# Optimization experiments

Measured on AMD Instinct MI355X. Metric: run time of the kernel, lower is better.

## Reference

```python
import jax, jax.numpy as jnp
import numpy as np

H_HEADS = 8
DIM_HEAD = 64


def setup_inputs() -> dict:
    key = jax.random.key(0)
    ks = jax.random.split(key, 5)
    b, c, Hs, Ws = 16, 32, 128, 128
    qd = H_HEADS * c              # 256 (heads*c = Linear in_features)
    inner = H_HEADS * DIM_HEAD    # 512
    s = 0.02                      # keep logits in a sane range
    return {
        "x": jax.random.normal(ks[0], (b, c, Hs, Ws), jnp.float32),
        "Wq": jax.random.normal(ks[1], (inner, qd), jnp.float32) * s,
        "Wkv": jax.random.normal(ks[2], (2 * inner, qd), jnp.float32) * s,
        "Wout": jax.random.normal(ks[3], (qd, inner), jnp.float32) * s,
        "bout": jax.random.normal(ks[4], (qd,), jnp.float32) * s,
    }


def _proj(arg, W, bias=None):
    # apply_operator_or_ffn for nn.Linear:
    # rearrange '(b h) n d -> b d (h n)', Linear over last dim, then 'b d n -> b n d'
    B, n, d = arg.shape
    bp = B // H_HEADS
    t = arg.reshape(bp, H_HEADS, n, d)
    t = jnp.transpose(t, (0, 3, 1, 2)).reshape(bp, d, H_HEADS * n)  # [b', d, h*n]
    y = t @ W.T
    if bias is not None:
        y = y + bias
    return jnp.transpose(y, (0, 2, 1))  # [b', out_features, d]


def _split_heads(t):
    # 'b (h d) n -> (b h) d n'
    bp, hd, n = t.shape
    return t.reshape(bp, H_HEADS, hd // H_HEADS, n).reshape(bp * H_HEADS, hd // H_HEADS, n)


def reference(x, Wq, Wkv, Wout, bout):
    b, c = x.shape[0], x.shape[1]
    spatial = x.shape[2:]
    N = int(np.prod(spatial))
    scale = DIM_HEAD ** -0.5
    xf = x.reshape(b, c, N)
    q = _proj(xf, Wq)              # [b/h, inner, N]
    kv = _proj(xf, Wkv)            # [b/h, 2*inner, N]
    inner = q.shape[1]
    k, v = kv[:, :inner], kv[:, inner:]
    qh, kh, vh = _split_heads(q), _split_heads(k), _split_heads(v)  # [b, DIM_HEAD, N]
    sim = jnp.einsum('bin,bjn->bij', qh, kh) * scale                 # [b, dh, dh]
    attn = jax.nn.softmax(sim, axis=-1)
    out = jnp.einsum('bnj,bjd->bnd', attn, vh)                       # [b, dh, N]
    out = _proj(out, Wout, bout)                                     # [b/h, h*c, N]
    return out.reshape(b, c, *spatial)
```

## Files before the change

### kernel.cpp

```cpp
#include <hip/hip_runtime.h>
#include <cstdint>
#include <cstddef>

using u16 = unsigned short;
using u32 = unsigned int;

typedef __attribute__((ext_vector_type(8))) short bf16x8;
typedef __attribute__((ext_vector_type(16))) float f32x16;

__device__ __forceinline__ u16 f2bf(float f) {
  union { float f; u32 i; } x; x.f = f;
  u32 r = (x.i + 0x7FFFu + ((x.i >> 16) & 1u)) >> 16;
  return (u16)r;
}
__device__ __forceinline__ bf16x8 ldbf16x8(const u16* p) {
  union { uint4 u; bf16x8 v; } t;
  t.u = *(const uint4*)p;
  return t.v;
}

constexpr int NP = 16384;


constexpr size_t OFF_C   = 0;
constexpr size_t OFF_T   = 131072;
constexpr size_t OFF_AT  = 393216;
constexpr size_t OFF_WE  = 458752;
constexpr size_t OFF_MT  = 720896;
constexpr size_t OFF_MA  = 851968;
constexpr size_t OFF_XB  = 917504;
constexpr size_t OFF_XBT = 5111808;
constexpr size_t OFF_CP1 = 9306112;
constexpr size_t NEED1   = (OFF_CP1 + 2097152) * 4;
constexpr size_t OFF_CP2 = 851968;
constexpr size_t NEED2   = (OFF_CP2 + 6291456) * 4;

__global__ __launch_bounds__(256)
void k0_cvt(const float* __restrict__ x, u16* __restrict__ XbF,
            u16* __restrict__ XbTF) {
  __shared__ float Fs[256 * 65];
  const int pc = blockIdx.x;
  const int g  = blockIdx.y;
  const int p0 = pc * 64;
  const float* __restrict__ Xg = x + (size_t)g * 256 * NP;
  u16* __restrict__ XbFg  = XbF  + (size_t)g * 256 * NP;
  u16* __restrict__ XbTFg = XbTF + (size_t)g * NP * 256;
  const int tid = threadIdx.x;
  const int f8i = tid & 7, rb = tid >> 3;
  const int sA = pc * 4 + (f8i >> 1);
  const int hA = f8i & 1;
  for (int pass = 0; pass < 8; ++pass) {
    const int row = rb + pass * 32;
    const size_t e0 = (size_t)row * NP + p0 + f8i * 8;
    float4 a = *(const float4*)(Xg + e0);
    float4 b = *(const float4*)(Xg + e0 + 4);
    const float v[8] = {a.x, a.y, a.z, a.w, b.x, b.y, b.z, b.w};
    uint4 s;
    s.x = (u32)f2bf(v[0]) | ((u32)f2bf(v[1]) << 16);
    s.y = (u32)f2bf(v[2]) | ((u32)f2bf(v[3]) << 16);
    s.z = (u32)f2bf(v[4]) | ((u32)f2bf(v[5]) << 16);
    s.w = (u32)f2bf(v[6]) | ((u32)f2bf(v[7]) << 16);
    const int panel = row >> 5, lc = row & 31;
    *(uint4*)(XbFg + (size_t)panel * 524288 + sA * 512 + hA * 256 + lc * 8) = s;
    float* d = &Fs[row * 65 + f8i * 8];
#pragma unroll
    for (int e = 0; e < 8; ++e) d[e] = v[e];
  }
  __syncthreads();
  const int p = tid & 63, grp = tid >> 6;
  const int pp = p0 + p;
  const int panelT = pp >> 5, lcT = pp & 31;
  u16* dstT = XbTFg + (size_t)panelT * 8192 + lcT * 8;
  for (int c = 0; c < 4; ++c) {
    const int sT = grp * 4 + c;
    u32 w[8];
#pragma unroll
    for (int q = 0; q < 8; ++q) {
      const int f = grp * 64 + c * 16 + q * 2;
      u32 lo = f2bf(Fs[f * 65 + p]);
      u32 hi = f2bf(Fs[(f + 1) * 65 + p]);
      w[q] = lo | (hi << 16);
    }
    uint4 s0 = {w[0], w[1], w[2], w[3]};
    uint4 s1 = {w[4], w[5], w[6], w[7]};
    *(uint4*)(dstT + sT * 512)       = s0;
    *(uint4*)(dstT + sT * 512 + 256) = s1;
  }
}

__global__ __launch_bounds__(256)
void k1_mfma(const u16* __restrict__ XbF, float* __restrict__ Cpart) {
  const int kc = blockIdx.x;
  const int tp = blockIdx.y;
  const int g  = blockIdx.z;
  const int ti = tp >> 2, tj = tp & 3;
  const int tid = threadIdx.x;
  const int w = tid >> 6, half = (tid >> 5) & 1, lc = tid & 31;
  const int qi = w >> 1, qj = w & 1;
  const u16* __restrict__ Xg = XbF + (size_t)g * 256 * NP;
  const u16* A = Xg + (size_t)(ti * 2 + qi) * 524288 + (size_t)kc * 32768 +
                 half * 256 + lc * 8;
  const u16* B = Xg + (size_t)(tj * 2 + qj) * 524288 + (size_t)kc * 32768 +
                 half * 256 + lc * 8;
  f32x16 acc;
#pragma unroll
  for (int i = 0; i < 16; ++i) acc[i] = 0.f;
#pragma unroll 4
  for (int s = 0; s < 64; ++s) {
    bf16x8 a = ldbf16x8(A + s * 512);
    bf16x8 b = ldbf16x8(B + s * 512);
    acc = __builtin_amdgcn_mfma_f32_32x32x16_bf16(a, b, acc, 0, 0, 0);
  }
  float* __restrict__ P = Cpart + (((size_t)g * 16 + tp) * 16 + kc) * 4096;
#pragma unroll
  for (int r = 0; r < 16; ++r) {
    const int row = qi * 32 + (r & 3) + 8 * (r >> 2) + 4 * half;
    const int col = qj * 32 + lc;
    P[row * 64 + col] = acc[r];
  }
}

__global__ __launch_bounds__(256)
void k1b_red(const float* __restrict__ Cpart, float* __restrict__ Cmat) {
  const int sl = blockIdx.x;
  const int tp = blockIdx.y;
  const int g  = blockIdx.z;
  const int ele = sl * 256 + threadIdx.x;
  const float* __restrict__ P =
      Cpart + (((size_t)g * 16 + tp) * 16) * 4096 + ele;
  float v = 0.f;
#pragma unroll
  for (int kc = 0; kc < 16; ++kc) v += P[(size_t)kc * 4096];
  const int ti = tp >> 2, tj = tp & 3;
  const int r64 = ele >> 6, c64 = ele & 63;
  Cmat[(size_t)g * 65536 + (size_t)(ti * 64 + r64) * 256 + tj * 64 + c64] = v;
}

__global__ __launch_bounds__(256)
void k1_gram(const float* __restrict__ x, float* __restrict__ Cpart) {
  __shared__ float As[32 * 132];
  __shared__ float Bs[32 * 132];
  const int kc = blockIdx.x, ty = blockIdx.y, g = blockIdx.z;
  const int i0 = (ty == 2) ? 128 : 0;
  const int j0 = (ty == 0) ? 0 : 128;
  const float* __restrict__ Xg = x + (size_t)g * 256 * NP;
  const int tid = threadIdx.x, lane = tid & 63, w = tid >> 6;
  const int wy = (w >> 1) * 64, wx = (w & 1) * 64;
  const int ly = (lane >> 3) * 8, lx = (lane & 7) * 8;
  float acc[8][8];
#pragma unroll
  for (int e = 0; e < 8; ++e)
#pragma unroll
    for (int f = 0; f < 8; ++f) acc[e][f] = 0.f;
  const int k8 = (tid & 3) * 8, rowb = tid >> 2, k0 = kc * 256;
  for (int s = 0; s < 8; ++s) {
    const int ks = k0 + s * 32;
#pragma unroll
    for (int pass = 0; pass < 2; ++pass) {
      const int row = rowb + pass * 64;
      const size_t ea = (size_t)(i0 + row) * NP + ks + k8;
      float4 a = *(const float4*)(Xg + ea);
      float4 b = *(const float4*)(Xg + ea + 4);
      As[(k8+0)*132+row]=a.x; As[(k8+1)*132+row]=a.y;
      As[(k8+2)*132+row]=a.z; As[(k8+3)*132+row]=a.w;
      As[(k8+4)*132+row]=b.x; As[(k8+5)*132+row]=b.y;
      As[(k8+6)*132+row]=b.z; As[(k8+7)*132+row]=b.w;
      const size_t eb = (size_t)(j0 + row) * NP + ks + k8;
      a = *(const float4*)(Xg + eb);
      b = *(const float4*)(Xg + eb + 4);
      Bs[(k8+0)*132+row]=a.x; Bs[(k8+1)*132+row]=a.y;
      Bs[(k8+2)*132+row]=a.z; Bs[(k8+3)*132+row]=a.w;
      Bs[(k8+4)*132+row]=b.x; Bs[(k8+5)*132+row]=b.y;
      Bs[(k8+6)*132+row]=b.z; Bs[(k8+7)*132+row]=b.w;
    }
    __syncthreads();
#pragma unroll 4
    for (int kk = 0; kk < 32; ++kk) {
      const float* ar = &As[kk * 132 + wy + ly];
      const float* br = &Bs[kk * 132 + wx + lx];
      float4 a0 = *(const float4*)(ar), a1 = *(const float4*)(ar + 4);
      float4 b0 = *(const float4*)(br), b1 = *(const float4*)(br + 4);
      const float av[8] = {a0.x,a0.y,a0.z,a0.w,a1.x,a1.y,a1.z,a1.w};
      const float bv[8] = {b0.x,b0.y,b0.z,b0.w,b1.x,b1.y,b1.z,b1.w};
#pragma unroll
      for (int e = 0; e < 8; ++e)
#pragma unroll
        for (int f = 0; f < 8; ++f) acc[e][f] += av[e] * bv[f];
    }
    __syncthreads();
  }
  float* __restrict__ P = Cpart + (((size_t)g * 3 + ty) * 64 + kc) * 16384;
#pragma unroll
  for (int e = 0; e < 8; ++e) {
    float* pr = P + (size_t)(wy + ly + e) * 128 + wx + lx;
    float4 s0 = {acc[e][0], acc[e][1], acc[e][2], acc[e][3]};
    float4 s1 = {acc[e][4], acc[e][5], acc[e][6], acc[e][7]};
    *(float4*)(pr)     = s0;
    *(float4*)(pr + 4) = s1;
  }
}

__global__ __launch_bounds__(256)
void k1b_reduce(const float* __restrict__ Cpart, float* __restrict__ Cmat) {
  const int sl = blockIdx.x, ty = blockIdx.y, g = blockIdx.z;
  const int ele = sl * 256 + threadIdx.x;
  const float* __restrict__ P =
      Cpart + (((size_t)g * 3 + ty) * 64) * 16384 + ele;
  float v = 0.f;
#pragma unroll 8
  for (int kc = 0; kc < 64; ++kc) v += P[(size_t)kc * 16384];
  const int i0 = (ty == 2) ? 128 : 0;
  const int j0 = (ty == 0) ? 0 : 128;
  const int i = ele >> 7, j = ele & 127;
  float* Cg = Cmat + (size_t)g * 65536;
  Cg[(size_t)(i0 + i) * 256 + (j0 + j)] = v;
  if (ty == 1) Cg[(size_t)(j0 + j) * 256 + (i0 + i)] = v;
}

__global__ __launch_bounds__(256)
void k1_gram_atomic(const float* __restrict__ x, float* __restrict__ Cmat) {
  __shared__ float As[32 * 132];
  __shared__ float Bs[32 * 132];
  const int kc = blockIdx.x, ty = blockIdx.y, g = blockIdx.z;
  const int i0 = (ty == 2) ? 128 : 0;
  const int j0 = (ty == 0) ? 0 : 128;
  const float* __restrict__ Xg = x + (size_t)g * 256 * NP;
  const int tid = threadIdx.x, lane = tid & 63, w = tid >> 6;
  const int wy = (w >> 1) * 64, wx = (w & 1) * 64;
  const int ly = (lane >> 3) * 8, lx = (lane & 7) * 8;
  float acc[8][8];
#pragma unroll
  for (int e = 0; e < 8; ++e)
#pragma unroll
    for (int f = 0; f < 8; ++f) acc[e][f] = 0.f;
  const int k8 = (tid & 3) * 8, rowb = tid >> 2, k0 = kc * 256;
  for (int s = 0; s < 8; ++s) {
    const int ks = k0 + s * 32;
#pragma unroll
    for (int pass = 0; pass < 2; ++pass) {
      const int row = rowb + pass * 64;
      const size_t ea = (size_t)(i0 + row) * NP + ks + k8;
      float4 a = *(const float4*)(Xg + ea);
      float4 b = *(const float4*)(Xg + ea + 4);
      As[(k8+0)*132+row]=a.x; As[(k8+1)*132+row]=a.y;
      As[(k8+2)*132+row]=a.z; As[(k8+3)*132+row]=a.w;
      As[(k8+4)*132+row]=b.x; As[(k8+5)*132+row]=b.y;
      As[(k8+6)*132+row]=b.z; As[(k8+7)*132+row]=b.w;
      const size_t eb = (size_t)(j0 + row) * NP + ks + k8;
      a = *(const float4*)(Xg + eb);
      b = *(const float4*)(Xg + eb + 4);
      Bs[(k8+0)*132+row]=a.x; Bs[(k8+1)*132+row]=a.y;
      Bs[(k8+2)*132+row]=a.z; Bs[(k8+3)*132+row]=a.w;
      Bs[(k8+4)*132+row]=b.x; Bs[(k8+5)*132+row]=b.y;
      Bs[(k8+6)*132+row]=b.z; Bs[(k8+7)*132+row]=b.w;
    }
    __syncthreads();
#pragma unroll 4
    for (int kk = 0; kk < 32; ++kk) {
      const float* ar = &As[kk * 132 + wy + ly];
      const float* br = &Bs[kk * 132 + wx + lx];
      float4 a0 = *(const float4*)(ar), a1 = *(const float4*)(ar + 4);
      float4 b0 = *(const float4*)(br), b1 = *(const float4*)(br + 4);
      const float av[8] = {a0.x,a0.y,a0.z,a0.w,a1.x,a1.y,a1.z,a1.w};
      const float bv[8] = {b0.x,b0.y,b0.z,b0.w,b1.x,b1.y,b1.z,b1.w};
#pragma unroll
      for (int e = 0; e < 8; ++e)
#pragma unroll
        for (int f = 0; f < 8; ++f) acc[e][f] += av[e] * bv[f];
    }
    __syncthreads();
  }
  float* Cg = Cmat + (size_t)g * 65536;
#pragma unroll
  for (int e = 0; e < 8; ++e)
#pragma unroll
    for (int f = 0; f < 8; ++f) {
      atomicAdd(&Cg[(i0+wy+ly+e)*256 + (j0+wx+lx+f)], acc[e][f]);
      if (ty == 1)
        atomicAdd(&Cg[(j0+wx+lx+f)*256 + (i0+wy+ly+e)], acc[e][f]);
    }
}

__global__ __launch_bounds__(256)
void kA_attn(const float* __restrict__ Wq, const float* __restrict__ Wkv,
             const float* __restrict__ Cmat, float* __restrict__ attn) {
  __shared__ float WqL[4 * 256];
  __shared__ float Ts[4 * 256];
  const int bh = blockIdx.x;
  const int ic = blockIdx.y;
  const int g = bh >> 3, hh = bh & 7;
  const int tid = threadIdx.x;
  const float* __restrict__ Cg = Cmat + (size_t)g * 65536;
  {
    const int r = tid >> 6, c4 = (tid & 63) * 4;
    *(float4*)(&WqL[r * 256 + c4]) =
        *(const float4*)(Wq + (size_t)(hh * 64 + ic * 4 + r) * 256 + c4);
  }
  __syncthreads();
  float acc[4] = {0.f, 0.f, 0.f, 0.f};
#pragma unroll 8
  for (int b = 0; b < 256; ++b) {
    const float cv = Cg[(size_t)b * 256 + tid];
#pragma unroll
    for (int r = 0; r < 4; ++r) acc[r] += WqL[r * 256 + b] * cv;
  }
#pragma unroll
  for (int r = 0; r < 4; ++r) Ts[r * 256 + tid] = acc[r];
  __syncthreads();
  const int r = tid >> 6, j = tid & 63;
  const float* __restrict__ Wk = Wkv + (size_t)(hh * 64 + j) * 256;
  float s = 0.f;
#pragma unroll 4
  for (int a4 = 0; a4 < 64; ++a4) {
    float4 w = *(const float4*)(Wk + a4 * 4);
    const float* t4 = &Ts[r * 256 + a4 * 4];
    s += t4[0] * w.x + t4[1] * w.y + t4[2] * w.z + t4[3] * w.w;
  }
  s *= 0.125f;
  float m = s;
#pragma unroll
  for (int off = 32; off; off >>= 1) m = fmaxf(m, __shfl_xor(m, off));
  const float e = __expf(s - m);
  float sum = e;
#pragma unroll
  for (int off = 32; off; off >>= 1) sum += __shfl_xor(sum, off);
  attn[((size_t)bh * 64 + ic * 4 + r) * 64 + j] = e / sum;
}

__global__ __launch_bounds__(256)
void kB_m(const float* __restrict__ Wout, const float* __restrict__ Wkv,
          const float* __restrict__ attn, float* __restrict__ Mp) {
  __shared__ float AtL[64 * 64];
  __shared__ float WoL[16 * 64];
  __shared__ float UL[16 * 64];
  const int bh = blockIdx.x;
  const int cc = blockIdx.y;
  const int g = bh >> 3, hh = bh & 7;
  const int tid = threadIdx.x;
  {
    const float* __restrict__ A = attn + (size_t)bh * 4096;
#pragma unroll
    for (int q = 0; q < 4; ++q)
      *(float4*)(&AtL[q * 1024 + tid * 4]) =
          *(const float4*)(A + q * 1024 + tid * 4);
  }
  {
    const int co_l = tid >> 4, i4 = (tid & 15) * 4;
    *(float4*)(&WoL[co_l * 64 + i4]) =
        *(const float4*)(Wout + (size_t)(cc * 16 + co_l) * 512 + hh * 64 + i4);
  }
  __syncthreads();
  const int j = tid & 63, cw = tid >> 6;
  float u4[4] = {0.f, 0.f, 0.f, 0.f};
#pragma unroll 4
  for (int i = 0; i < 64; ++i) {
    const float av = AtL[i * 64 + j];
#pragma unroll
    for (int u = 0; u < 4; ++u) u4[u] += WoL[(cw * 4 + u) * 64 + i] * av;
  }
  __syncthreads();
#pragma unroll
  for (int u = 0; u < 4; ++u) UL[(cw * 4 + u) * 64 + j] = u4[u];
  __syncthreads();
  float acc[16];
#pragma unroll
  for (int c = 0; c < 16; ++c) acc[c] = 0.f;
#pragma unroll 4
  for (int j2 = 0; j2 < 64; ++j2) {
    const float wv = Wkv[(size_t)(512 + hh * 64 + j2) * 256 + tid];
#pragma unroll
    for (int c = 0; c < 16; ++c) acc[c] += UL[c * 64 + j2] * wv;
  }
  float* __restrict__ P =
      Mp + (((size_t)g * 8 + hh) * 256 + cc * 16) * 256 + tid;
#pragma unroll
  for (int c = 0; c < 16; ++c) P[(size_t)c * 256] = acc[c];
}

__global__ __launch_bounds__(256)
void kC_red(const float* __restrict__ Mp, u16* __restrict__ MA) {
  const int panel = blockIdx.x;
  const int g     = blockIdx.y;
  const int tid = threadIdx.x;
  const float* __restrict__ Pg = Mp + (size_t)g * 8 * 65536;
  u16* __restrict__ Mg = MA + (size_t)g * 65536;
#pragma unroll
  for (int q = 0; q < 4; ++q) {
    const int item = tid + q * 256;
    const int lc = item & 31;
    const int co = panel * 32 + lc;
    const int b0 = (item >> 5) * 8;
    float v[8] = {0.f, 0.f, 0.f, 0.f, 0.f, 0.f, 0.f, 0.f};
#pragma unroll
    for (int hd = 0; hd < 8; ++hd) {
      const float* p = Pg + (size_t)hd * 65536 + (size_t)co * 256 + b0;
      float4 a = *(const float4*)(p);
      float4 b = *(const float4*)(p + 4);
      v[0] += a.x; v[1] += a.y; v[2] += a.z; v[3] += a.w;
      v[4] += b.x; v[5] += b.y; v[6] += b.z; v[7] += b.w;
    }
    uint4 sdat;
    sdat.x = (u32)f2bf(v[0]) | ((u32)f2bf(v[1]) << 16);
    sdat.y = (u32)f2bf(v[2]) | ((u32)f2bf(v[3]) << 16);
    sdat.z = (u32)f2bf(v[4]) | ((u32)f2bf(v[5]) << 16);
    sdat.w = (u32)f2bf(v[6]) | ((u32)f2bf(v[7]) << 16);
    *(uint4*)(Mg + (size_t)panel * 8192 + (size_t)item * 8) = sdat;
  }
}

__global__ __launch_bounds__(256) void k2_T(const float* __restrict__ Wq,
                                            const float* __restrict__ Cmat,
                                            float* __restrict__ T) {
  const int bh = blockIdx.x;
  const int ic = blockIdx.y;
  const int g = bh >> 3, hh = bh & 7;
  const int tid = threadIdx.x;
  const float* __restrict__ Cg = Cmat + (size_t)g * 65536;
  const int r0 = hh * 64 + ic * 4;
  float acc[4] = {0.f, 0.f, 0.f, 0.f};
#pragma unroll 8
  for (int b = 0; b < 256; ++b) {
    const float cv = Cg[(size_t)b * 256 + tid];
#pragma unroll
    for (int ii = 0; ii < 4; ++ii)
      acc[ii] += Wq[(size_t)(r0 + ii) * 256 + b] * cv;
  }
#pragma unroll
  for (int ii = 0; ii < 4; ++ii)
    T[((size_t)bh * 64 + ic * 4 + ii) * 256 + tid] = acc[ii];
}

__global__ __launch_bounds__(256) void k3_sim(const float* __restrict__ Wkv,
                                              const float* __restrict__ T,
                                              float* __restrict__ simattn) {
  __shared__ float Ts[64 * 256];
  const int bh = blockIdx.x;
  const int jc = blockIdx.y;
  const int hh = bh & 7;
  const int tid = threadIdx.x;
  {
    const int f4i = tid & 63;
    const int rwb = tid >> 6;
    for (int pass = 0; pass < 16; ++pass) {
      const int row = rwb + pass * 4;
      float4 v = *(const float4*)(T + ((size_t)bh * 64 + row) * 256 + f4i * 4);
      const int a0 = f4i * 4;
      const float vv[4] = {v.x, v.y, v.z, v.w};
#pragma unroll
      for (int e = 0; e < 4; ++e) {
        const int a = a0 + e;
        Ts[row * 256 + (a & ~31) + ((a + row) & 31)] = vv[e];
      }
    }
  }
  __syncthreads();
  const int i  = tid & 63;
  const int jq = tid >> 6;
  const int jb = jc * 16 + jq * 4;
  float acc[4] = {0.f, 0.f, 0.f, 0.f};
#pragma unroll 4
  for (int a = 0; a < 256; ++a) {
    const float tv = Ts[i * 256 + (a & ~31) + ((a + i) & 31)];
#pragma unroll
    for (int jj = 0; jj < 4; ++jj)
      acc[jj] += Wkv[(size_t)(hh * 64 + jb + jj) * 256 + a] * tv;
  }
#pragma unroll
  for (int jj = 0; jj < 4; ++jj)
    simattn[((size_t)bh * 64 + i) * 64 + jb + jj] = acc[jj] * 0.125f;
}

__global__ __launch_bounds__(64) void k3b_softmax(float* __restrict__ simattn) {
  const int bh = blockIdx.x;
  const int i  = threadIdx.x;
  float* row = simattn + ((size_t)bh * 64 + i) * 64;
  float v[64];
  float m = -1e30f;
#pragma unroll
  for (int j = 0; j < 64; ++j) { v[j] = row[j]; m = fmaxf(m, v[j]); }
  float s = 0.f;
#pragma unroll
  for (int j = 0; j < 64; ++j) { v[j] = __expf(v[j] - m); s += v[j]; }
  const float inv = 1.0f / s;
#pragma unroll
  for (int j = 0; j < 64; ++j) row[j] = v[j] * inv;
}

__global__ __launch_bounds__(256) void k4_we(const float* __restrict__ Wout,
                                             const float* __restrict__ attn,
                                             float* __restrict__ WeT) {
  __shared__ float WL[256 * 64];
  const int jc = blockIdx.x;
  const int hh = blockIdx.y;
  const int g  = blockIdx.z;
  const int bh = g * 8 + hh;
  const int tid = threadIdx.x;
  {
    const int f4i = tid & 15;
    const int cb  = tid >> 4;
    for (int pass = 0; pass < 16; ++pass) {
      const int co = cb + pass * 16;
      float4 v = *(const float4*)(Wout + (size_t)co * 512 + hh * 64 + f4i * 4);
      const int a0 = f4i * 4;
      const float vv[4] = {v.x, v.y, v.z, v.w};
#pragma unroll
      for (int e = 0; e < 4; ++e)
        WL[co * 64 + ((a0 + e + co) & 63)] = vv[e];
    }
  }
  __syncthreads();
  const int jb = jc * 8;
  float acc[8] = {0.f, 0.f, 0.f, 0.f, 0.f, 0.f, 0.f, 0.f};
#pragma unroll 4
  for (int i = 0; i < 64; ++i) {
    const float wv = WL[tid * 64 + ((i + tid) & 63)];
#pragma unroll
    for (int je = 0; je < 8; ++je)
      acc[je] += attn[((size_t)bh * 64 + i) * 64 + jb + je] * wv;
  }
#pragma unroll
  for (int je = 0; je < 8; ++je)
    WeT[(size_t)g * 131072 + (size_t)(hh * 64 + jb + je) * 256 + tid] =
        acc[je];
}

__global__ __launch_bounds__(256)
void k5a_part(const float* __restrict__ Wkv, const float* __restrict__ WeT,
              float* __restrict__ Mp) {
  const int bc = blockIdx.x;
  const int oc = blockIdx.y;
  const int g  = blockIdx.z;
  const int tid = threadIdx.x;
  const int b0 = bc * 4;
  const float* __restrict__ Weg = WeT + (size_t)g * 131072;
  float acc[4] = {0.f, 0.f, 0.f, 0.f};
#pragma unroll 8
  for (int u = 0; u < 32; ++u) {
    const int o = oc * 32 + u;
    const float wv = Weg[(size_t)o * 256 + tid];
    const float* __restrict__ vr = Wkv + (size_t)(512 + o) * 256 + b0;
    acc[0] += vr[0] * wv;
    acc[1] += vr[1] * wv;
    acc[2] += vr[2] * wv;
    acc[3] += vr[3] * wv;
  }
#pragma unroll
  for (int be = 0; be < 4; ++be)
    Mp[(((size_t)g * 16 + oc) * 256 + b0 + be) * 256 + tid] = acc[be];
}

__global__ __launch_bounds__(256)
void k5b_red(const float* __restrict__ Mp, float* __restrict__ Mt,
             u16* __restrict__ MA) {
  const int b = blockIdx.x;
  const int g = blockIdx.y;
  const int tid = threadIdx.x;
  const float* __restrict__ P =
      Mp + ((size_t)g * 16 * 256 + b) * 256 + tid;
  float v = 0.f;
#pragma unroll
  for (int oc = 0; oc < 16; ++oc) v += P[(size_t)oc * 65536];
  Mt[(size_t)g * 65536 + (size_t)b * 256 + tid] = v;
  MA[(size_t)g * 65536 + (size_t)tid * 256 + b] = f2bf(v);
}

__global__ __launch_bounds__(256) void k5_serial(const float* __restrict__ Wkv,
                                                 const float* __restrict__ WeT,
                                                 float* __restrict__ Mt,
                                                 u16* __restrict__ MA) {
  const int bc = blockIdx.x;
  const int g  = blockIdx.y;
  const int tid = threadIdx.x;
  const int b0 = bc * 4;
  const float* __restrict__ Weg = WeT + (size_t)g * 131072;
  float acc[4] = {0.f, 0.f, 0.f, 0.f};
#pragma unroll 4
  for (int o = 0; o < 512; ++o) {
    const float wv = Weg[(size_t)o * 256 + tid];
    const float* __restrict__ vr = Wkv + (size_t)(512 + o) * 256 + b0;
    acc[0] += vr[0] * wv;
    acc[1] += vr[1] * wv;
    acc[2] += vr[2] * wv;
    acc[3] += vr[3] * wv;
  }
#pragma unroll
  for (int be = 0; be < 4; ++be) {
    Mt[(size_t)g * 65536 + (size_t)(b0 + be) * 256 + tid] = acc[be];
    MA[(size_t)g * 65536 + (size_t)tid * 256 + b0 + be] = f2bf(acc[be]);
  }
}

__global__ __launch_bounds__(256)
void k6_mfma(const u16* __restrict__ XbTF, const u16* __restrict__ MA,
             const float* __restrict__ bout, float* __restrict__ out) {
  const int pb = blockIdx.x;
  const int cb = blockIdx.y;
  const int g  = blockIdx.z;
  const int tid = threadIdx.x;
  const int w = tid >> 6, half = (tid >> 5) & 1, lc = tid & 31;
  const int p0  = pb * 128 + w * 32;
  const int co0 = cb * 128;
  const u16* __restrict__ Ap = XbTF + (size_t)g * NP * 256 +
                               (size_t)(pb * 4 + w) * 8192 + half * 256 +
                               lc * 8;
  const u16* __restrict__ Bp = MA + (size_t)g * 65536 +
                               (size_t)cb * 32768 + half * 256 + lc * 8;
  f32x16 acc[4];
#pragma unroll
  for (int t = 0; t < 4; ++t)
#pragma unroll
    for (int i = 0; i < 16; ++i) acc[t][i] = 0.f;
#pragma unroll 2
  for (int s = 0; s < 16; ++s) {
    bf16x8 a = ldbf16x8(Ap + s * 512);
#pragma unroll
    for (int t = 0; t < 4; ++t) {
      bf16x8 b = ldbf16x8(Bp + (size_t)t * 8192 + s * 512);
      acc[t] = __builtin_amdgcn_mfma_f32_32x32x16_bf16(a, b, acc[t], 0, 0, 0);
    }
  }
#pragma unroll
  for (int t = 0; t < 4; ++t) {
    const int co = co0 + t * 32 + lc;
    const float bo = bout[co];
    float* __restrict__ ocol =
        out + ((size_t)(g * 256 + co)) * NP + p0 + 4 * half;
#pragma unroll
    for (int rg = 0; rg < 4; ++rg) {
      float4 v = {acc[t][rg * 4 + 0] + bo, acc[t][rg * 4 + 1] + bo,
                  acc[t][rg * 4 + 2] + bo, acc[t][rg * 4 + 3] + bo};
      *(float4*)(ocol + rg * 8) = v;
    }
  }
}

__global__ __launch_bounds__(256)
void k6_apply(const float* __restrict__ x, const float* __restrict__ Mt,
              const float* __restrict__ bout, float* __restrict__ out) {
  __shared__ float As[32 * 132];
  __shared__ float Bs[32 * 132];
  const int pc = blockIdx.x;
  const int oy = blockIdx.y;
  const int g  = blockIdx.z;
  const int p0 = pc * 128;
  const int o0 = oy * 128;
  const float* __restrict__ Xg = x + (size_t)g * 256 * NP;
  const float* __restrict__ Mg = Mt + (size_t)g * 65536;
  const int tid  = threadIdx.x;
  const int lane = tid & 63;
  const int w    = tid >> 6;
  const int wy = (w >> 1) * 64;
  const int wx = (w & 1) * 64;
  const int ly = (lane >> 3) * 8;
  const int lx = (lane & 7) * 8;
  float acc[8][8];
#pragma unroll
  for (int e = 0; e < 8; ++e)
#pragma unroll
    for (int f = 0; f < 8; ++f) acc[e][f] = 0.f;
  const int c4 = (tid & 31) * 4;
  const int kb = tid >> 5;
  for (int s = 0; s < 8; ++s) {
#pragma unroll
    for (int r = 0; r < 4; ++r) {
      const int kk = kb + r * 8;
      const int f  = s * 32 + kk;
      *(float4*)&As[kk * 132 + c4] =
          *(const float4*)(Mg + (size_t)f * 256 + o0 + c4);
      *(float4*)&Bs[kk * 132 + c4] =
          *(const float4*)(Xg + (size_t)f * NP + p0 + c4);
    }
    __syncthreads();
#pragma unroll 4
    for (int kk = 0; kk < 32; ++kk) {
      const float* __restrict__ ar = &As[kk * 132 + wy + ly];
      const float* __restrict__ br = &Bs[kk * 132 + wx + lx];
      float4 a0 = *(const float4*)(ar);
      float4 a1 = *(const float4*)(ar + 4);
      float4 b0 = *(const float4*)(br);
      float4 b1 = *(const float4*)(br + 4);
      const float av[8] = {a0.x, a0.y, a0.z, a0.w, a1.x, a1.y, a1.z, a1.w};
      const float bv[8] = {b0.x, b0.y, b0.z, b0.w, b1.x, b1.y, b1.z, b1.w};
#pragma unroll
      for (int e = 0; e < 8; ++e)
#pragma unroll
        for (int f = 0; f < 8; ++f) acc[e][f] += av[e] * bv[f];
    }
    __syncthreads();
  }
#pragma unroll
  for (int e = 0; e < 8; ++e) {
    const int co = o0 + wy + ly + e;
    const float bo = bout[co];
    float* __restrict__ orow =
        out + ((size_t)(g * 256 + co)) * NP + p0 + wx + lx;
    float4 s0 = {acc[e][0] + bo, acc[e][1] + bo, acc[e][2] + bo,
                 acc[e][3] + bo};
    float4 s1 = {acc[e][4] + bo, acc[e][5] + bo, acc[e][6] + bo,
                 acc[e][7] + bo};
    *(float4*)(orow)     = s0;
    *(float4*)(orow + 4) = s1;
  }
}

extern "C" void kernel_launch(void* const* d_in, const int* in_sizes, int n_in,
                              void* d_out, int out_size, void* d_ws,
                              size_t ws_size, hipStream_t stream) {
  const float* x    = (const float*)d_in[0];
  const float* Wq   = (const float*)d_in[1];
  const float* Wkv  = (const float*)d_in[2];
  const float* Wout = (const float*)d_in[3];
  const float* bout = (const float*)d_in[4];
  float* out = (float*)d_out;
  float* ws  = (float*)d_ws;

  float* C    = ws + OFF_C;
  float* T    = ws + OFF_T;
  float* att  = ws + OFF_AT;
  float* WeT  = ws + OFF_WE;
  float* Mt   = ws + OFF_MT;
  u16*   MA   = (u16*)(ws + OFF_MA);
  u16*   Xb   = (u16*)(ws + OFF_XB);
  u16*   XbT  = (u16*)(ws + OFF_XBT);
  float* Cp1  = ws + OFF_CP1;
  float* Cp2  = ws + OFF_CP2;

  const bool mfma_path = (ws_size >= NEED1);
  const bool splitk    = (ws_size >= NEED2);

  if (mfma_path) {
    k0_cvt<<<dim3(256, 2), 256, 0, stream>>>(x, Xb, XbT);
    k1_mfma<<<dim3(16, 16, 2), 256, 0, stream>>>(Xb, Cp1);
    k1b_red<<<dim3(16, 16, 2), 256, 0, stream>>>(Cp1, C);
    kA_attn<<<dim3(16, 16), 256, 0, stream>>>(Wq, Wkv, C, att);
    kB_m<<<dim3(16, 16), 256, 0, stream>>>(Wout, Wkv, att, Cp1);
    kC_red<<<dim3(8, 2), 256, 0, stream>>>(Cp1, MA);
    k6_mfma<<<dim3(128, 2, 2), 256, 0, stream>>>(XbT, MA, bout, out);
    return;
  }

  if (splitk) {
    k1_gram<<<dim3(64, 3, 2), 256, 0, stream>>>(x, Cp2);
    k1b_reduce<<<dim3(64, 3, 2), 256, 0, stream>>>(Cp2, C);
  } else {
    hipMemsetAsync(C, 0, 131072 * sizeof(float), stream);
    k1_gram_atomic<<<dim3(64, 3, 2), 256, 0, stream>>>(x, C);
  }
  k2_T<<<dim3(16, 16), 256, 0, stream>>>(Wq, C, T);
  k3_sim<<<dim3(16, 4), 256, 0, stream>>>(Wkv, T, att);
  k3b_softmax<<<dim3(16), 64, 0, stream>>>(att);
  k4_we<<<dim3(8, 8, 2), 256, 0, stream>>>(Wout, att, WeT);
  if (splitk) {
    k5a_part<<<dim3(64, 16, 2), 256, 0, stream>>>(Wkv, WeT, Cp2);
    k5b_red<<<dim3(256, 2), 256, 0, stream>>>(Cp2, Mt, MA);
  } else {
    k5_serial<<<dim3(64, 2), 256, 0, stream>>>(Wkv, WeT, Mt, MA);
  }
  k6_apply<<<dim3(128, 2, 2), 256, 0, stream>>>(x, Mt, bout, out);
}
```

Baseline: 158.8 us.

## Enlarge Gram MFMA tiles to 128x128, stage bf16 transpose, spread kC_red blocks

The Gram-matrix MFMA kernel now has each wave compute a 2x2 block of 32x32 tiles, giving 128x128 output tiles per block with 32 K-chunks. This cuts redundant global loads of X panels, since each A/B fragment is reused twice, at the cost of a larger split-K partial buffer and a bigger workspace requirement. The conversion kernel stores already-rounded bf16 pairs in shared memory instead of floats, which halves LDS use and removes the repeated f2bf conversions in the transpose phase. kC_red is split across four times as many blocks to raise parallelism in that small reduction.

```diff
diff --git a/kernel.cpp b/kernel.cpp
--- a/kernel.cpp
+++ b/kernel.cpp
@@ -31,14 +31,14 @@
 constexpr size_t OFF_XB  = 917504;
 constexpr size_t OFF_XBT = 5111808;
 constexpr size_t OFF_CP1 = 9306112;
-constexpr size_t NEED1   = (OFF_CP1 + 2097152) * 4;
+constexpr size_t NEED1   = (OFF_CP1 + 4194304) * 4;
 constexpr size_t OFF_CP2 = 851968;
 constexpr size_t NEED2   = (OFF_CP2 + 6291456) * 4;
 
 __global__ __launch_bounds__(256)
 void k0_cvt(const float* __restrict__ x, u16* __restrict__ XbF,
             u16* __restrict__ XbTF) {
-  __shared__ float Fs[256 * 65];
+  __shared__ u32 Fs[256 * 33];
   const int pc = blockIdx.x;
   const int g  = blockIdx.y;
   const int p0 = pc * 64;
@@ -62,14 +62,14 @@
     s.w = (u32)f2bf(v[6]) | ((u32)f2bf(v[7]) << 16);
     const int panel = row >> 5, lc = row & 31;
     *(uint4*)(XbFg + (size_t)panel * 524288 + sA * 512 + hA * 256 + lc * 8) = s;
-    float* d = &Fs[row * 65 + f8i * 8];
-#pragma unroll
-    for (int e = 0; e < 8; ++e) d[e] = v[e];
+    u32* d = &Fs[row * 33 + f8i * 4];
+    d[0] = s.x; d[1] = s.y; d[2] = s.z; d[3] = s.w;
   }
   __syncthreads();
   const int p = tid & 63, grp = tid >> 6;
   const int pp = p0 + p;
   const int panelT = pp >> 5, lcT = pp & 31;
+  const u16* __restrict__ Fs16 = (const u16*)Fs;
   u16* dstT = XbTFg + (size_t)panelT * 8192 + lcT * 8;
   for (int c = 0; c < 4; ++c) {
     const int sT = grp * 4 + c;
@@ -77,8 +77,8 @@
 #pragma unroll
     for (int q = 0; q < 8; ++q) {
       const int f = grp * 64 + c * 16 + q * 2;
-      u32 lo = f2bf(Fs[f * 65 + p]);
-      u32 hi = f2bf(Fs[(f + 1) * 65 + p]);
+      u32 lo = Fs16[f * 66 + p];
+      u32 hi = Fs16[(f + 1) * 66 + p];
       w[q] = lo | (hi << 16);
     }
     uint4 s0 = {w[0], w[1], w[2], w[3]};
@@ -90,33 +90,44 @@
 
 __global__ __launch_bounds__(256)
 void k1_mfma(const u16* __restrict__ XbF, float* __restrict__ Cpart) {
-  const int kc = blockIdx.x;
-  const int tp = blockIdx.y;
+  const int tp = blockIdx.x;
+  const int kc = blockIdx.y;
   const int g  = blockIdx.z;
-  const int ti = tp >> 2, tj = tp & 3;
+  const int ti = tp >> 1, tj = tp & 1;
   const int tid = threadIdx.x;
   const int w = tid >> 6, half = (tid >> 5) & 1, lc = tid & 31;
   const int qi = w >> 1, qj = w & 1;
   const u16* __restrict__ Xg = XbF + (size_t)g * 256 * NP;
-  const u16* A = Xg + (size_t)(ti * 2 + qi) * 524288 + (size_t)kc * 32768 +
-                 half * 256 + lc * 8;
-  const u16* B = Xg + (size_t)(tj * 2 + qj) * 524288 + (size_t)kc * 32768 +
-                 half * 256 + lc * 8;
-  f32x16 acc;
-#pragma unroll
-  for (int i = 0; i < 16; ++i) acc[i] = 0.f;
-#pragma unroll 4
-  for (int s = 0; s < 64; ++s) {
-    bf16x8 a = ldbf16x8(A + s * 512);
-    bf16x8 b = ldbf16x8(B + s * 512);
-    acc = __builtin_amdgcn_mfma_f32_32x32x16_bf16(a, b, acc, 0, 0, 0);
-  }
-  float* __restrict__ P = Cpart + (((size_t)g * 16 + tp) * 16 + kc) * 4096;
+  const size_t koff = (size_t)kc * 16384 + half * 256 + lc * 8;
+  const u16* A0 = Xg + (size_t)(ti * 4 + qi * 2 + 0) * 524288 + koff;
+  const u16* A1 = Xg + (size_t)(ti * 4 + qi * 2 + 1) * 524288 + koff;
+  const u16* B0 = Xg + (size_t)(tj * 4 + qj * 2 + 0) * 524288 + koff;
+  const u16* B1 = Xg + (size_t)(tj * 4 + qj * 2 + 1) * 524288 + koff;
+  f32x16 acc00, acc01, acc10, acc11;
+#pragma unroll
+  for (int i = 0; i < 16; ++i) {
+    acc00[i] = 0.f; acc01[i] = 0.f; acc10[i] = 0.f; acc11[i] = 0.f;
+  }
+#pragma unroll 4
+  for (int s = 0; s < 32; ++s) {
+    bf16x8 a0 = ldbf16x8(A0 + s * 512);
+    bf16x8 a1 = ldbf16x8(A1 + s * 512);
+    bf16x8 b0 = ldbf16x8(B0 + s * 512);
+    bf16x8 b1 = ldbf16x8(B1 + s * 512);
+    acc00 = __builtin_amdgcn_mfma_f32_32x32x16_bf16(a0, b0, acc00, 0, 0, 0);
+    acc01 = __builtin_amdgcn_mfma_f32_32x32x16_bf16(a0, b1, acc01, 0, 0, 0);
+    acc10 = __builtin_amdgcn_mfma_f32_32x32x16_bf16(a1, b0, acc10, 0, 0, 0);
+    acc11 = __builtin_amdgcn_mfma_f32_32x32x16_bf16(a1, b1, acc11, 0, 0, 0);
+  }
+  float* __restrict__ P = Cpart + (((size_t)g * 4 + tp) * 32 + kc) * 16384;
 #pragma unroll
   for (int r = 0; r < 16; ++r) {
-    const int row = qi * 32 + (r & 3) + 8 * (r >> 2) + 4 * half;
-    const int col = qj * 32 + lc;
-    P[row * 64 + col] = acc[r];
+    const int rr = (r & 3) + 8 * (r >> 2) + 4 * half;
+    const int row0 = qi * 64 + rr, col0 = qj * 64 + lc;
+    P[(row0 +  0) * 128 + col0 +  0] = acc00[r];
+    P[(row0 +  0) * 128 + col0 + 32] = acc01[r];
+    P[(row0 + 32) * 128 + col0 +  0] = acc10[r];
+    P[(row0 + 32) * 128 + col0 + 32] = acc11[r];
   }
 }
 
@@ -127,13 +138,13 @@
   const int g  = blockIdx.z;
   const int ele = sl * 256 + threadIdx.x;
   const float* __restrict__ P =
-      Cpart + (((size_t)g * 16 + tp) * 16) * 4096 + ele;
+      Cpart + (((size_t)g * 4 + tp) * 32) * 16384 + ele;
   float v = 0.f;
 #pragma unroll
-  for (int kc = 0; kc < 16; ++kc) v += P[(size_t)kc * 4096];
-  const int ti = tp >> 2, tj = tp & 3;
-  const int r64 = ele >> 6, c64 = ele & 63;
-  Cmat[(size_t)g * 65536 + (size_t)(ti * 64 + r64) * 256 + tj * 64 + c64] = v;
+  for (int kc = 0; kc < 32; ++kc) v += P[(size_t)kc * 16384];
+  const int ti = tp >> 1, tj = tp & 1;
+  const int i = ele >> 7, j = ele & 127;
+  Cmat[(size_t)g * 65536 + (size_t)(ti * 128 + i) * 256 + tj * 128 + j] = v;
 }
 
 __global__ __launch_bounds__(256)
@@ -379,33 +390,31 @@
 
 __global__ __launch_bounds__(256)
 void kC_red(const float* __restrict__ Mp, u16* __restrict__ MA) {
-  const int panel = blockIdx.x;
+  const int panel = blockIdx.x >> 2;
+  const int q     = blockIdx.x & 3;
   const int g     = blockIdx.y;
   const int tid = threadIdx.x;
   const float* __restrict__ Pg = Mp + (size_t)g * 8 * 65536;
   u16* __restrict__ Mg = MA + (size_t)g * 65536;
-#pragma unroll
-  for (int q = 0; q < 4; ++q) {
-    const int item = tid + q * 256;
-    const int lc = item & 31;
-    const int co = panel * 32 + lc;
-    const int b0 = (item >> 5) * 8;
-    float v[8] = {0.f, 0.f, 0.f, 0.f, 0.f, 0.f, 0.f, 0.f};
-#pragma unroll
-    for (int hd = 0; hd < 8; ++hd) {
-      const float* p = Pg + (size_t)hd * 65536 + (size_t)co * 256 + b0;
-      float4 a = *(const float4*)(p);
-      float4 b = *(const float4*)(p + 4);
-      v[0] += a.x; v[1] += a.y; v[2] += a.z; v[3] += a.w;
-      v[4] += b.x; v[5] += b.y; v[6] += b.z; v[7] += b.w;
-    }
-    uint4 sdat;
-    sdat.x = (u32)f2bf(v[0]) | ((u32)f2bf(v[1]) << 16);
-    sdat.y = (u32)f2bf(v[2]) | ((u32)f2bf(v[3]) << 16);
-    sdat.z = (u32)f2bf(v[4]) | ((u32)f2bf(v[5]) << 16);
-    sdat.w = (u32)f2bf(v[6]) | ((u32)f2bf(v[7]) << 16);
-    *(uint4*)(Mg + (size_t)panel * 8192 + (size_t)item * 8) = sdat;
-  }
+  const int item = tid + q * 256;
+  const int lc = item & 31;
+  const int co = panel * 32 + lc;
+  const int b0 = (item >> 5) * 8;
+  float v[8] = {0.f, 0.f, 0.f, 0.f, 0.f, 0.f, 0.f, 0.f};
+#pragma unroll
+  for (int hd = 0; hd < 8; ++hd) {
+    const float* p = Pg + (size_t)hd * 65536 + (size_t)co * 256 + b0;
+    float4 a = *(const float4*)(p);
+    float4 b = *(const float4*)(p + 4);
+    v[0] += a.x; v[1] += a.y; v[2] += a.z; v[3] += a.w;
+    v[4] += b.x; v[5] += b.y; v[6] += b.z; v[7] += b.w;
+  }
+  uint4 sdat;
+  sdat.x = (u32)f2bf(v[0]) | ((u32)f2bf(v[1]) << 16);
+  sdat.y = (u32)f2bf(v[2]) | ((u32)f2bf(v[3]) << 16);
+  sdat.z = (u32)f2bf(v[4]) | ((u32)f2bf(v[5]) << 16);
+  sdat.w = (u32)f2bf(v[6]) | ((u32)f2bf(v[7]) << 16);
+  *(uint4*)(Mg + (size_t)panel * 8192 + (size_t)item * 8) = sdat;
 }
 
 __global__ __launch_bounds__(256) void k2_T(const float* __restrict__ Wq,
@@ -730,11 +739,11 @@
 
   if (mfma_path) {
     k0_cvt<<<dim3(256, 2), 256, 0, stream>>>(x, Xb, XbT);
-    k1_mfma<<<dim3(16, 16, 2), 256, 0, stream>>>(Xb, Cp1);
-    k1b_red<<<dim3(16, 16, 2), 256, 0, stream>>>(Cp1, C);
+    k1_mfma<<<dim3(4, 32, 2), 256, 0, stream>>>(Xb, Cp1);
+    k1b_red<<<dim3(64, 4, 2), 256, 0, stream>>>(Cp1, C);
     kA_attn<<<dim3(16, 16), 256, 0, stream>>>(Wq, Wkv, C, att);
     kB_m<<<dim3(16, 16), 256, 0, stream>>>(Wout, Wkv, att, Cp1);
-    kC_red<<<dim3(8, 2), 256, 0, stream>>>(Cp1, MA);
+    kC_red<<<dim3(32, 2), 256, 0, stream>>>(Cp1, MA);
     k6_mfma<<<dim3(128, 2, 2), 256, 0, stream>>>(XbT, MA, bout, out);
     return;
   }
```

Result: no change. 159.3 us (+0.3%).
